# Kernel tuning notes

Hardware: AMD Instinct MI355X
Metric: run time of the kernel (lower is better)

Reference implementation:

```python
import jax, jax.numpy as jnp
import numpy as np

M_CHECKS = 256      # check nodes
DC = 16             # variables per check (check degree)
NEURONS = M_CHECKS * DC  # 4096 Tanner-graph edges
BATCH = 1024
EPS = 1e-8


def build_mask():
    # edge id = check*DC + t ; mask[j, i] = 1 iff same check, different variable
    block = np.ones((DC, DC), np.float32) - np.eye(DC, dtype=np.float32)
    return jnp.asarray(np.kron(np.eye(M_CHECKS, dtype=np.float32), block))


def setup_inputs() -> dict:
    key = jax.random.key(0)
    k1, k2 = jax.random.split(key)
    # tanh-domain variable-to-check messages, |x| < ~1 (keeps exp(sum log|x|) stable)
    x = 0.25 * jax.random.normal(k1, (BATCH, NEURONS), dtype=jnp.float32)
    mask = build_mask()
    # learned weights initialized near 1 (weighted-BP init)
    even_weights = 1.0 + 0.02 * jax.random.normal(k2, (NEURONS, NEURONS), dtype=jnp.float32)
    return {"x": x, "even_weights": even_weights, "w_even2odd_mask": mask}


def reference(x, even_weights, w_even2odd_mask):
    log_abs_x = jnp.log(jnp.abs(x) + EPS)                       # [B, E]
    x_b = 0.5 - 0.5 * jnp.sign(x)                               # hard bits
    syndrome = jnp.mod(x_b @ w_even2odd_mask, 2.0)              # [B, E]
    bipolar_syndrome = 1.0 - 2.0 * syndrome
    log_abs_x_tanner = log_abs_x @ (w_even2odd_mask * even_weights)
    even_prod_messages = bipolar_syndrome * jnp.exp(log_abs_x_tanner)
    return jnp.log((1.0 + even_prod_messages + EPS) / (1.0 - even_prod_messages + EPS))
```

## Files before the change

### kernel.cpp

```cpp
#include <hip/hip_runtime.h>


constexpr int M_CHECKS = 256;
constexpr int DC = 16;
constexpr int NEURONS = M_CHECKS * DC;
constexpr int BATCH = 1024;
constexpr float EPS = 1e-8f;

__global__ __launch_bounds__(256) void even_layer_kernel(
    const float* __restrict__ x,
    const float* __restrict__ w,
    float* __restrict__ out)
{
    __shared__ float Wsh[DC][DC];

    const int c     = blockIdx.x & (M_CHECKS - 1);
    const int chunk = blockIdx.x >> 8;
    const int tid   = (int)threadIdx.x;
    const int bi    = tid >> 4;
    const int i     = tid & 15;

    {
        const int j = bi;
        float wv = w[(size_t)(c * DC + j) * NEURONS + (size_t)(c * DC + i)];
        Wsh[j][i] = (j == i) ? 0.0f : wv;
    }
    __syncthreads();

    const int lane  = tid & 63;
    const int gbase = lane & 48;

    #pragma unroll
    for (int p = 0; p < 4; ++p) {
        const int b = chunk * 64 + p * 16 + bi;
        const size_t idx = (size_t)b * NEURONS + (size_t)(c * DC + i);

        const float xv = x[idx];
        const float la = logf(fabsf(xv) + EPS);
        const int bit = (xv < 0.0f) ? 1 : 0;

        const unsigned long long m = __ballot(bit);
        int par = __popcll((m >> gbase) & 0xFFFFull) & 1;
        par ^= bit;

        float dot = 0.0f;
        #pragma unroll
        for (int jj = 0; jj < DC; ++jj) {
            const float lav = __shfl(la, gbase + jj, 64);
            dot = fmaf(lav, Wsh[jj][i], dot);
        }

        const float e = expf(dot);
        const float even = par ? -e : e;
        const float r = logf((1.0f + even + EPS) / (1.0f - even + EPS));
        out[idx] = r;
    }
}

extern "C" void kernel_launch(void* const* d_in, const int* in_sizes, int n_in,
                              void* d_out, int out_size, void* d_ws, size_t ws_size,
                              hipStream_t stream) {
    const float* x = (const float*)d_in[0];
    const float* w = (const float*)d_in[1];
    float* out = (float*)d_out;

    dim3 grid(M_CHECKS * (BATCH / 64));
    dim3 block(256);
    hipLaunchKernelGGL(even_layer_kernel, grid, block, 0, stream, x, w, out);
}
```

Before: 21.13 us.

## Assign one check row per thread with float4 loads and register-local dot

Each thread now owns a whole check node for one batch row. It loads its 16 messages with float4 vector loads, works out the parity from a local bitmask, and computes all 16 outputs in registers using float4 weight reads from padded shared memory. This replaces the per-element wave ballot and 16 shuffles, and the grid becomes 16 checks by 16 batch rows per block. Global accesses become strided per thread (a 64-byte span per thread), and per-thread register use rises with the la and acc arrays.

```diff
diff --git a/kernel.cpp b/kernel.cpp
--- a/kernel.cpp
+++ b/kernel.cpp
@@ -7,54 +7,115 @@
 constexpr int BATCH = 1024;
 constexpr float EPS = 1e-8f;
 
+constexpr int CB = 16;
+constexpr int BB = 16;
+constexpr int BS4 = 65;
+
 __global__ __launch_bounds__(256) void even_layer_kernel(
     const float* __restrict__ x,
     const float* __restrict__ w,
     float* __restrict__ out)
 {
-    __shared__ float Wsh[DC][DC];
+    __shared__ float4 Wsh[CB * BS4];
 
-    const int c     = blockIdx.x & (M_CHECKS - 1);
-    const int chunk = blockIdx.x >> 8;
-    const int tid   = (int)threadIdx.x;
-    const int bi    = tid >> 4;
-    const int i     = tid & 15;
+    const int tid = (int)threadIdx.x;
+    const int cb  = (int)blockIdx.x & 15;
+    const int bb  = (int)blockIdx.x >> 4;
 
     {
-        const int j = bi;
-        float wv = w[(size_t)(c * DC + j) * NEURONS + (size_t)(c * DC + i)];
-        Wsh[j][i] = (j == i) ? 0.0f : wv;
+        const int cl = tid >> 4;
+        const int j  = tid & 15;
+        const int c  = cb * CB + cl;
+        const float* src = w + (size_t)(c * DC + j) * NEURONS + (size_t)(c * DC);
+        #pragma unroll
+        for (int k = 0; k < 4; ++k) {
+            float4 v = *(const float4*)(src + 4 * k);
+            if ((j >> 2) == k) {
+                if ((j & 3) == 0) v.x = 0.0f;
+                else if ((j & 3) == 1) v.y = 0.0f;
+                else if ((j & 3) == 2) v.z = 0.0f;
+                else v.w = 0.0f;
+            }
+            Wsh[cl * BS4 + j * 4 + k] = v;
+        }
     }
     __syncthreads();
 
-    const int lane  = tid & 63;
-    const int gbase = lane & 48;
+    const int bi = tid >> 4;
+    const int ci = tid & 15;
+    const int b  = bb * BB + bi;
+    const int c  = cb * CB + ci;
+
+    const float* xp = x + (size_t)b * NEURONS + (size_t)(c * DC);
+
+    float la[DC];
+    int sbits = 0;
+
+    #define LOADPROC(XV, J)                                   \
+        { const float xv_ = (XV);                             \
+          la[J] = logf(fabsf(xv_) + EPS);                     \
+          if (xv_ < 0.0f) sbits |= (1 << (J)); }
 
     #pragma unroll
-    for (int p = 0; p < 4; ++p) {
-        const int b = chunk * 64 + p * 16 + bi;
-        const size_t idx = (size_t)b * NEURONS + (size_t)(c * DC + i);
+    for (int k = 0; k < 4; ++k) {
+        const float4 v = *(const float4*)(xp + 4 * k);
+        LOADPROC(v.x, 4 * k + 0)
+        LOADPROC(v.y, 4 * k + 1)
+        LOADPROC(v.z, 4 * k + 2)
+        LOADPROC(v.w, 4 * k + 3)
+    }
+    const int sall = __popc(sbits) & 1;
 
-        const float xv = x[idx];
-        const float la = logf(fabsf(xv) + EPS);
-        const int bit = (xv < 0.0f) ? 1 : 0;
+    float acc[DC];
+    #pragma unroll
+    for (int i = 0; i < DC; ++i) acc[i] = 0.0f;
 
-        const unsigned long long m = __ballot(bit);
-        int par = __popcll((m >> gbase) & 0xFFFFull) & 1;
-        par ^= bit;
+    const int wbase = ci * BS4;
+    #pragma unroll
+    for (int j = 0; j < DC; ++j) {
+        const float lj = la[j];
+        const float4 w0 = Wsh[wbase + j * 4 + 0];
+        const float4 w1 = Wsh[wbase + j * 4 + 1];
+        const float4 w2 = Wsh[wbase + j * 4 + 2];
+        const float4 w3 = Wsh[wbase + j * 4 + 3];
+        acc[0]  = fmaf(lj, w0.x, acc[0]);
+        acc[1]  = fmaf(lj, w0.y, acc[1]);
+        acc[2]  = fmaf(lj, w0.z, acc[2]);
+        acc[3]  = fmaf(lj, w0.w, acc[3]);
+        acc[4]  = fmaf(lj, w1.x, acc[4]);
+        acc[5]  = fmaf(lj, w1.y, acc[5]);
+        acc[6]  = fmaf(lj, w1.z, acc[6]);
+        acc[7]  = fmaf(lj, w1.w, acc[7]);
+        acc[8]  = fmaf(lj, w2.x, acc[8]);
+        acc[9]  = fmaf(lj, w2.y, acc[9]);
+        acc[10] = fmaf(lj, w2.z, acc[10]);
+        acc[11] = fmaf(lj, w2.w, acc[11]);
+        acc[12] = fmaf(lj, w3.x, acc[12]);
+        acc[13] = fmaf(lj, w3.y, acc[13]);
+        acc[14] = fmaf(lj, w3.z, acc[14]);
+        acc[15] = fmaf(lj, w3.w, acc[15]);
+    }
 
-        float dot = 0.0f;
-        #pragma unroll
-        for (int jj = 0; jj < DC; ++jj) {
-            const float lav = __shfl(la, gbase + jj, 64);
-            dot = fmaf(lav, Wsh[jj][i], dot);
-        }
+    float* op = out + (size_t)b * NEURONS + (size_t)(c * DC);
 
-        const float e = expf(dot);
-        const float even = par ? -e : e;
-        const float r = logf((1.0f + even + EPS) / (1.0f - even + EPS));
-        out[idx] = r;
+    #define EPI(RCOMP, I)                                                   \
+        { const float e_ = expf(acc[I]);                                    \
+          const int par_ = sall ^ ((sbits >> (I)) & 1);                     \
+          const float even_ = par_ ? -e_ : e_;                              \
+          RCOMP = logf((1.0f + even_ + EPS) / (1.0f - even_ + EPS)); }
+
+    #pragma unroll
+    for (int k = 0; k < 4; ++k) {
+        float4 r;
+        EPI(r.x, 4 * k + 0)
+        EPI(r.y, 4 * k + 1)
+        EPI(r.z, 4 * k + 2)
+        EPI(r.w, 4 * k + 3)
+        *(float4*)(op + 4 * k) = r;
     }
+
+    #undef LOADPROC
+    #undef EPI
 }
 
 extern "C" void kernel_launch(void* const* d_in, const int* in_sizes, int n_in,
@@ -64,7 +125,7 @@
     const float* w = (const float*)d_in[1];
     float* out = (float*)d_out;
 
-    dim3 grid(M_CHECKS * (BATCH / 64));
+    dim3 grid((BATCH / BB) * (M_CHECKS / CB));
     dim3 block(256);
     hipLaunchKernelGGL(even_layer_kernel, grid, block, 0, stream, x, w, out);
 }
```

Result: faster. 17.81 us (-15.7%).
